# Kernel tuning notes

Hardware: AMD Instinct MI355X
Metric: run time of the kernel (lower is better)

Reference implementation:

```python
import jax, jax.numpy as jnp
import numpy as np

N = 8192
IN_F = 512
OUT_F = 256
POW = 2


def setup_inputs() -> dict:
    key = jax.random.key(0)
    k1, k2, k3, k4 = jax.random.split(key, 4)
    stdv = 1.0 / np.sqrt(OUT_F)
    inputs = {
        "input": jax.random.normal(k1, (N, IN_F), dtype=jnp.float32),
        "adj": jax.random.uniform(k2, (N, N), dtype=jnp.float32),
        "weight": jax.random.uniform(k3, (IN_F, OUT_F), dtype=jnp.float32, minval=-stdv, maxval=stdv),
        "bias": jax.random.uniform(k4, (OUT_F,), dtype=jnp.float32, minval=-stdv, maxval=stdv),
    }
    return inputs


def reference(input, adj, weight, bias):
    # K_adj = adj ** pow (elementwise power, as torch's ** on a dense tensor)
    k_adj = adj ** POW
    # support = X @ W  -> [N, out_features]
    support = jnp.einsum("ni,io->no", input, weight)
    # output = K_adj @ support -> [N, out_features]
    out = jnp.einsum("nm,mo->no", k_adj, support) + bias
    # F.elu with default alpha=1.0
    return jnp.where(out > 0, out, jnp.expm1(out))
```

## Files before the change

kernel.cpp:

```cpp
#include <hip/hip_runtime.h>
#include <cstdint>
#include <cstddef>

#define N_NODES 8192
#define INF 512
#define OUTF 256
#define SPLITK 8
#define MSLICE (N_NODES / SPLITK)

typedef _Float16 f16;
typedef _Float16 f16x8 __attribute__((ext_vector_type(8)));
typedef _Float16 f16x4 __attribute__((ext_vector_type(4)));
typedef float f32x4 __attribute__((ext_vector_type(4)));

__device__ __forceinline__ void async_copy16(void* lds_dst, const void* g_src) {
  __builtin_amdgcn_global_load_lds(
      (const __attribute__((address_space(1))) void*)g_src,
      (__attribute__((address_space(3))) void*)lds_dst,
      16, 0, 0);
}

__device__ __forceinline__ float elu(float x) { return x > 0.f ? x : expm1f(x); }

__global__ __launch_bounds__(256) void prep_w(const float* __restrict__ W,
                                              f16* __restrict__ WhT) {
  const int idx = blockIdx.x * 256 + threadIdx.x;
  const int o = idx >> 9, i = idx & 511;
  WhT[idx] = (f16)W[i * OUTF + o];
}

__global__ __launch_bounds__(256) void gemm1(const f16* __restrict__ WhT,
                                             const float* __restrict__ X,
                                             f16* __restrict__ supT) {
  __shared__ __align__(16) f16 Asm[64 * 64];
  __shared__ __align__(16) f16 Bsm[64 * 64];
  const int t = threadIdx.x;
  const int wave = t >> 6, lane = t & 63;
  const int q = lane >> 4, r = lane & 15;
  const int lrow = lane >> 3, lchunk = lane & 7;
  const int o0 = blockIdx.x * 64, m0 = blockIdx.y * 64;

  f32x4 acc[4];
#pragma unroll
  for (int i = 0; i < 4; ++i) acc[i] = (f32x4){0.f, 0.f, 0.f, 0.f};

  const int b_row = t >> 2;
  const int b_c0 = (t & 3) * 2;
  const float* xptr = X + (size_t)(m0 + b_row) * INF + (t & 3) * 16;

  for (int kt = 0; kt < 8; ++kt) {
    const int k0 = kt * 64;
#pragma unroll
    for (int op = 0; op < 2; ++op) {
      const int row = (wave * 2 + op) * 8 + lrow;
      const f16* src = WhT + (size_t)(o0 + row) * INF + k0 + (lchunk ^ lrow) * 8;
      async_copy16(Asm + (wave * 2 + op) * 512, src);
    }
    {
      const float* xp = xptr + k0;
      f32x4 v0 = *(const f32x4*)(xp + 0);
      f32x4 v1 = *(const f32x4*)(xp + 4);
      f32x4 v2 = *(const f32x4*)(xp + 8);
      f32x4 v3 = *(const f32x4*)(xp + 12);
      f16x8 h0, h1;
#pragma unroll
      for (int u = 0; u < 4; ++u) {
        h0[u] = (f16)v0[u];
        h0[4 + u] = (f16)v1[u];
        h1[u] = (f16)v2[u];
        h1[4 + u] = (f16)v3[u];
      }
      *(f16x8*)&Bsm[b_row * 64 + ((b_c0 ^ (b_row & 7)) * 8)] = h0;
      *(f16x8*)&Bsm[b_row * 64 + (((b_c0 + 1) ^ (b_row & 7)) * 8)] = h1;
    }
    __syncthreads();
#pragma unroll
    for (int s = 0; s < 2; ++s) {
      const int pc = ((s * 4 + q) ^ (r & 7)) * 8;
      f16x8 af[4];
#pragma unroll
      for (int i = 0; i < 4; ++i) af[i] = *(const f16x8*)&Asm[(i * 16 + r) * 64 + pc];
      const f16x8 bf = *(const f16x8*)&Bsm[(wave * 16 + r) * 64 + pc];
#pragma unroll
      for (int i = 0; i < 4; ++i)
        acc[i] = __builtin_amdgcn_mfma_f32_16x16x32_f16(af[i], bf, acc[i], 0, 0, 0);
    }
    __syncthreads();
  }
  const int m = m0 + wave * 16 + r;
#pragma unroll
  for (int i = 0; i < 4; ++i)
#pragma unroll
    for (int g = 0; g < 4; ++g)
      supT[(size_t)(o0 + i * 16 + q * 4 + g) * N_NODES + m] = (f16)acc[i][g];
}

template <bool ATOMIC>
__global__ __launch_bounds__(256, 4) void gemm2(const float* __restrict__ adj,
                                                const f16* __restrict__ supT,
                                                f16* __restrict__ P16,
                                                float* __restrict__ outp) {
  __shared__ __align__(16) f16 Asm[64 * 64];
  __shared__ __align__(16) f16 Bsm[256 * 64];
  const int t = threadIdx.x;
  const int wave = t >> 6, lane = t & 63;
  const int q = lane >> 4, r = lane & 15;
  const int n0 = blockIdx.x * 64;
  const size_t m_base = (size_t)blockIdx.y * MSLICE;

  f32x4 acc[4][4];
#pragma unroll
  for (int i = 0; i < 4; ++i)
#pragma unroll
    for (int j = 0; j < 4; ++j) acc[i][j] = (f32x4){0.f, 0.f, 0.f, 0.f};

  const int a_row = t >> 2;
  const int a_c0 = (t & 3) * 2;
  const float* aptr = adj + (size_t)(n0 + a_row) * N_NODES + m_base + (t & 3) * 16;
  const int b_o = wave * 64 + (lane >> 3);
  const int b_kb = lane & 7;

  for (int kt = 0; kt < MSLICE / 64; ++kt) {
#pragma unroll
    for (int j = 0; j < 8; ++j) {
      const int o = b_o + j * 8;
      const int kb = b_kb ^ (o & 7);
      const f16* src = supT + (size_t)o * N_NODES + m_base + kt * 64 + kb * 8;
      async_copy16(Bsm + (wave * 64 + j * 8) * 64, src);
    }
    {
      const float* ap = aptr + kt * 64;
      f32x4 v0 = *(const f32x4*)(ap + 0);
      f32x4 v1 = *(const f32x4*)(ap + 4);
      f32x4 v2 = *(const f32x4*)(ap + 8);
      f32x4 v3 = *(const f32x4*)(ap + 12);
      f16x8 h0, h1;
#pragma unroll
      for (int u = 0; u < 4; ++u) {
        h0[u] = (f16)(v0[u] * v0[u]);
        h0[4 + u] = (f16)(v1[u] * v1[u]);
        h1[u] = (f16)(v2[u] * v2[u]);
        h1[4 + u] = (f16)(v3[u] * v3[u]);
      }
      *(f16x8*)&Asm[a_row * 64 + ((a_c0 ^ (a_row & 7)) * 8)] = h0;
      *(f16x8*)&Asm[a_row * 64 + (((a_c0 + 1) ^ (a_row & 7)) * 8)] = h1;
    }
    __syncthreads();
#pragma unroll
    for (int s = 0; s < 2; ++s) {
      const int pc = ((s * 4 + q) ^ (r & 7)) * 8;
      f16x8 af[4], bf[4];
#pragma unroll
      for (int i = 0; i < 4; ++i) af[i] = *(const f16x8*)&Asm[(i * 16 + r) * 64 + pc];
#pragma unroll
      for (int j = 0; j < 4; ++j)
        bf[j] = *(const f16x8*)&Bsm[(wave * 64 + j * 16 + r) * 64 + pc];
#pragma unroll
      for (int i = 0; i < 4; ++i)
#pragma unroll
        for (int j = 0; j < 4; ++j)
          acc[i][j] = __builtin_amdgcn_mfma_f32_16x16x32_f16(af[i], bf[j],
                                                             acc[i][j], 0, 0, 0);
    }
    __syncthreads();
  }
  if (ATOMIC) {
#pragma unroll
    for (int i = 0; i < 4; ++i)
#pragma unroll
      for (int g = 0; g < 4; ++g) {
        const int n = n0 + i * 16 + q * 4 + g;
        float* orow = outp + (size_t)n * OUTF + wave * 64 + r;
#pragma unroll
        for (int j = 0; j < 4; ++j) atomicAdd(orow + j * 16, acc[i][j][g]);
      }
  } else {
    f16* base = P16 + (size_t)blockIdx.y * N_NODES * OUTF;
#pragma unroll
    for (int i = 0; i < 4; ++i)
#pragma unroll
      for (int g = 0; g < 4; ++g) {
        const int n = n0 + i * 16 + q * 4 + g;
        f16* orow = base + (size_t)n * OUTF + wave * 64 + r;
#pragma unroll
        for (int j = 0; j < 4; ++j) orow[j * 16] = (f16)acc[i][j][g];
      }
  }
}

__global__ __launch_bounds__(256) void reduce_elu(const f16* __restrict__ P16,
                                                  const float* __restrict__ bias,
                                                  float* __restrict__ out) {
  const int idx = blockIdx.x * 256 + threadIdx.x;
  f32x4 s = (f32x4){0.f, 0.f, 0.f, 0.f};
#pragma unroll
  for (int y = 0; y < SPLITK; ++y) {
    const f16x4 h = ((const f16x4*)(P16 + (size_t)y * N_NODES * OUTF))[idx];
#pragma unroll
    for (int u = 0; u < 4; ++u) s[u] += (float)h[u];
  }
  const f32x4 b = ((const f32x4*)bias)[idx & 63];
  f32x4 v;
#pragma unroll
  for (int u = 0; u < 4; ++u) v[u] = elu(s[u] + b[u]);
  ((f32x4*)out)[idx] = v;
}

__global__ __launch_bounds__(256) void bias_elu(float* __restrict__ out,
                                                const float* __restrict__ bias) {
  const int idx = blockIdx.x * 256 + threadIdx.x;
  f32x4 v = ((const f32x4*)out)[idx];
  const f32x4 b = ((const f32x4*)bias)[idx & 63];
#pragma unroll
  for (int u = 0; u < 4; ++u) v[u] = elu(v[u] + b[u]);
  ((f32x4*)out)[idx] = v;
}

extern "C" void kernel_launch(void* const* d_in, const int* in_sizes, int n_in,
                              void* d_out, int out_size, void* d_ws, size_t ws_size,
                              hipStream_t stream) {
  const float* X = (const float*)d_in[0];
  const float* adj = (const float*)d_in[1];
  const float* W = (const float*)d_in[2];
  const float* bias = (const float*)d_in[3];
  float* out = (float*)d_out;

  char* ws = (char*)d_ws;
  f16* supT = (f16*)(ws + 0);
  f16* WhT = (f16*)(ws + (4u << 20));
  f16* P16 = (f16*)(ws + (8u << 20));
  const size_t need = (40u << 20);

  prep_w<<<INF * OUTF / 256, 256, 0, stream>>>(W, WhT);
  gemm1<<<dim3(OUTF / 64, N_NODES / 64), 256, 0, stream>>>(WhT, X, supT);
  if (ws_size >= need) {
    gemm2<false><<<dim3(N_NODES / 64, SPLITK), 256, 0, stream>>>(adj, supT, P16, nullptr);
    reduce_elu<<<N_NODES * OUTF / 4 / 256, 256, 0, stream>>>(P16, bias, out);
  } else {
    hipMemsetAsync(d_out, 0, (size_t)out_size * sizeof(float), stream);
    gemm2<true><<<dim3(N_NODES / 64, SPLITK), 256, 0, stream>>>(adj, supT, nullptr, out);
    bias_elu<<<N_NODES * OUTF / 4 / 256, 256, 0, stream>>>(out, bias);
  }
}
```

Before: 435.1 us.

## Enlarge gemm2 tile to 128 rows with 512 threads and widen reduce

The adjacency GEMM block grows from 64 to 128 output rows with eight waves arranged 2x4, so each supT tile loaded into LDS is shared by twice as many rows, halving B traffic per output. The grid is flattened so that the split-K index varies fastest across consecutive blocks. The reduce kernel also handles 8 fp16 values per thread instead of 4. In exchange LDS per block grows and fewer blocks are launched, which may lower occupancy; launch_bounds(512,4) may force register pressure.

```diff
diff --git a/kernel.cpp b/kernel.cpp
--- a/kernel.cpp
+++ b/kernel.cpp
@@ -7,6 +7,7 @@
 #define OUTF 256
 #define SPLITK 8
 #define MSLICE (N_NODES / SPLITK)
+#define BN2 128
 
 typedef _Float16 f16;
 typedef _Float16 f16x8 __attribute__((ext_vector_type(8)));
@@ -96,17 +97,20 @@
 }
 
 template <bool ATOMIC>
-__global__ __launch_bounds__(256, 4) void gemm2(const float* __restrict__ adj,
+__global__ __launch_bounds__(512, 4) void gemm2(const float* __restrict__ adj,
                                                 const f16* __restrict__ supT,
                                                 f16* __restrict__ P16,
                                                 float* __restrict__ outp) {
-  __shared__ __align__(16) f16 Asm[64 * 64];
+  __shared__ __align__(16) f16 Asm[BN2 * 64];
   __shared__ __align__(16) f16 Bsm[256 * 64];
   const int t = threadIdx.x;
   const int wave = t >> 6, lane = t & 63;
   const int q = lane >> 4, r = lane & 15;
-  const int n0 = blockIdx.x * 64;
-  const size_t m_base = (size_t)blockIdx.y * MSLICE;
+  const int wn = wave >> 2, wo = wave & 3;
+  const int wg = blockIdx.x;
+  const int y = wg & 7;
+  const int n0 = (wg >> 3) * BN2;
+  const size_t m_base = (size_t)y * MSLICE;
 
   f32x4 acc[4][4];
 #pragma unroll
@@ -117,16 +121,17 @@
   const int a_row = t >> 2;
   const int a_c0 = (t & 3) * 2;
   const float* aptr = adj + (size_t)(n0 + a_row) * N_NODES + m_base + (t & 3) * 16;
-  const int b_o = wave * 64 + (lane >> 3);
+  const int b_o8 = lane >> 3;
   const int b_kb = lane & 7;
 
   for (int kt = 0; kt < MSLICE / 64; ++kt) {
 #pragma unroll
-    for (int j = 0; j < 8; ++j) {
-      const int o = b_o + j * 8;
+    for (int j = 0; j < 4; ++j) {
+      const int c = wave * 4 + j;
+      const int o = c * 8 + b_o8;
       const int kb = b_kb ^ (o & 7);
       const f16* src = supT + (size_t)o * N_NODES + m_base + kt * 64 + kb * 8;
-      async_copy16(Bsm + (wave * 64 + j * 8) * 64, src);
+      async_copy16(Bsm + c * 8 * 64, src);
     }
     {
       const float* ap = aptr + kt * 64;
@@ -151,10 +156,11 @@
       const int pc = ((s * 4 + q) ^ (r & 7)) * 8;
       f16x8 af[4], bf[4];
 #pragma unroll
-      for (int i = 0; i < 4; ++i) af[i] = *(const f16x8*)&Asm[(i * 16 + r) * 64 + pc];
+      for (int i = 0; i < 4; ++i)
+        af[i] = *(const f16x8*)&Asm[(wn * 64 + i * 16 + r) * 64 + pc];
 #pragma unroll
       for (int j = 0; j < 4; ++j)
-        bf[j] = *(const f16x8*)&Bsm[(wave * 64 + j * 16 + r) * 64 + pc];
+        bf[j] = *(const f16x8*)&Bsm[(wo * 64 + j * 16 + r) * 64 + pc];
 #pragma unroll
       for (int i = 0; i < 4; ++i)
 #pragma unroll
@@ -169,19 +175,19 @@
     for (int i = 0; i < 4; ++i)
 #pragma unroll
       for (int g = 0; g < 4; ++g) {
-        const int n = n0 + i * 16 + q * 4 + g;
-        float* orow = outp + (size_t)n * OUTF + wave * 64 + r;
+        const int n = n0 + wn * 64 + i * 16 + q * 4 + g;
+        float* orow = outp + (size_t)n * OUTF + wo * 64 + r;
 #pragma unroll
         for (int j = 0; j < 4; ++j) atomicAdd(orow + j * 16, acc[i][j][g]);
       }
   } else {
-    f16* base = P16 + (size_t)blockIdx.y * N_NODES * OUTF;
+    f16* base = P16 + (size_t)y * N_NODES * OUTF;
 #pragma unroll
     for (int i = 0; i < 4; ++i)
 #pragma unroll
       for (int g = 0; g < 4; ++g) {
-        const int n = n0 + i * 16 + q * 4 + g;
-        f16* orow = base + (size_t)n * OUTF + wave * 64 + r;
+        const int n = n0 + wn * 64 + i * 16 + q * 4 + g;
+        f16* orow = base + (size_t)n * OUTF + wo * 64 + r;
 #pragma unroll
         for (int j = 0; j < 4; ++j) orow[j * 16] = (f16)acc[i][j][g];
       }
@@ -192,18 +198,24 @@
                                                   const float* __restrict__ bias,
                                                   float* __restrict__ out) {
   const int idx = blockIdx.x * 256 + threadIdx.x;
-  f32x4 s = (f32x4){0.f, 0.f, 0.f, 0.f};
+  float s[8];
+#pragma unroll
+  for (int u = 0; u < 8; ++u) s[u] = 0.f;
 #pragma unroll
   for (int y = 0; y < SPLITK; ++y) {
-    const f16x4 h = ((const f16x4*)(P16 + (size_t)y * N_NODES * OUTF))[idx];
-#pragma unroll
-    for (int u = 0; u < 4; ++u) s[u] += (float)h[u];
-  }
-  const f32x4 b = ((const f32x4*)bias)[idx & 63];
-  f32x4 v;
-#pragma unroll
-  for (int u = 0; u < 4; ++u) v[u] = elu(s[u] + b[u]);
-  ((f32x4*)out)[idx] = v;
+    const f16x8 h = ((const f16x8*)(P16 + (size_t)y * N_NODES * OUTF))[idx];
+#pragma unroll
+    for (int u = 0; u < 8; ++u) s[u] += (float)h[u];
+  }
+  const float* bp = bias + (idx & 31) * 8;
+  f32x4 v0, v1;
+#pragma unroll
+  for (int u = 0; u < 4; ++u) {
+    v0[u] = elu(s[u] + bp[u]);
+    v1[u] = elu(s[4 + u] + bp[4 + u]);
+  }
+  ((f32x4*)out)[idx * 2 + 0] = v0;
+  ((f32x4*)out)[idx * 2 + 1] = v1;
 }
 
 __global__ __launch_bounds__(256) void bias_elu(float* __restrict__ out,
@@ -234,11 +246,11 @@
   prep_w<<<INF * OUTF / 256, 256, 0, stream>>>(W, WhT);
   gemm1<<<dim3(OUTF / 64, N_NODES / 64), 256, 0, stream>>>(WhT, X, supT);
   if (ws_size >= need) {
-    gemm2<false><<<dim3(N_NODES / 64, SPLITK), 256, 0, stream>>>(adj, supT, P16, nullptr);
-    reduce_elu<<<N_NODES * OUTF / 4 / 256, 256, 0, stream>>>(P16, bias, out);
+    gemm2<false><<<dim3((N_NODES / BN2) * SPLITK), dim3(512), 0, stream>>>(adj, supT, P16, nullptr);
+    reduce_elu<<<N_NODES * OUTF / 8 / 256, 256, 0, stream>>>(P16, bias, out);
   } else {
     hipMemsetAsync(d_out, 0, (size_t)out_size * sizeof(float), stream);
-    gemm2<true><<<dim3(N_NODES / 64, SPLITK), 256, 0, stream>>>(adj, supT, nullptr, out);
+    gemm2<true><<<dim3((N_NODES / BN2) * SPLITK), dim3(512), 0, stream>>>(adj, supT, nullptr, out);
     bias_elu<<<N_NODES * OUTF / 4 / 256, 256, 0, stream>>>(out, bias);
   }
 }
```

New measurement: 417.9 us. 4.0% less time.
